# Optimization experiments

Hardware: AMD Instinct MI355X
Metric: run time of the kernel (lower is better)

Reference implementation:

```python
import jax, jax.numpy as jnp
import numpy as np

N_NODES = 100000
N_EDGES = 1600000
D_IN, D_H, D_OUT = 256, 128, 128


def setup_inputs() -> dict:
    key = jax.random.key(0)
    ks = jax.random.split(key, 8)
    x = jax.random.normal(ks[0], (N_NODES, D_IN), dtype=jnp.float32)
    edge_index = jax.random.randint(ks[1], (2, N_EDGES), 0, N_NODES, dtype=jnp.int64)
    def glorot(k, fan_in, fan_out):
        s = jnp.sqrt(6.0 / (fan_in + fan_out))
        return jax.random.uniform(k, (fan_in, fan_out), jnp.float32, -s, s)
    W1 = glorot(ks[2], D_IN, D_H)
    b1 = jnp.zeros((D_H,), jnp.float32)
    W2 = glorot(ks[3], D_H, D_H)
    b2 = jnp.zeros((D_H,), jnp.float32)
    W3 = glorot(ks[4], D_H, D_OUT)
    b3 = jnp.zeros((D_OUT,), jnp.float32)
    return {"x": x, "edge_index": edge_index,
            "W1": W1, "b1": b1, "W2": W2, "b2": b2, "W3": W3, "b3": b3}


def _gcn_norm(edge_index, n_nodes):
    # PyG GCNConv: add self-loops, symmetric normalization D^-1/2 (A+I) D^-1/2
    loop = jnp.arange(n_nodes, dtype=edge_index.dtype)
    src = jnp.concatenate([edge_index[0], loop])  # source j
    dst = jnp.concatenate([edge_index[1], loop])  # target i
    deg = jax.ops.segment_sum(jnp.ones_like(dst, dtype=jnp.float32), dst,
                              num_segments=n_nodes)
    dinv = jnp.where(deg > 0, jax.lax.rsqrt(deg), 0.0)
    norm = dinv[src] * dinv[dst]  # [E+N]
    return src, dst, norm


def _gcn_conv(h, W, b, src, dst, norm, n_nodes):
    h = h @ W                                   # [N, d_out] transform first
    msg = h[src] * norm[:, None]                # gather + edge-weight
    out = jax.ops.segment_sum(msg, dst, num_segments=n_nodes)  # scatter-add
    return out + b


def reference(x, edge_index, W1, b1, W2, b2, W3, b3):
    n = x.shape[0]
    src, dst, norm = _gcn_norm(edge_index, n)
    h = jax.nn.relu(_gcn_conv(x, W1, b1, src, dst, norm, n))
    h = jax.nn.relu(_gcn_conv(h, W2, b2, src, dst, norm, n))
    return _gcn_conv(h, W3, b3, src, dst, norm, n)
```

## Files before the change

### kernel.cpp

```cpp
#include <hip/hip_runtime.h>
#include <hip/hip_fp16.h>
#include <math.h>


#define N_NODES 100000
#define N_EDGES 1600000

typedef _Float16 f16x8 __attribute__((ext_vector_type(8)));
typedef float    f32x4 __attribute__((ext_vector_type(4)));


__global__ __launch_bounds__(256) void k_zero_int(int* __restrict__ p, int n) {
    int i = blockIdx.x * 256 + threadIdx.x;
    if (i < n) p[i] = 0;
}

__global__ __launch_bounds__(256) void k_count(const int* __restrict__ dst, int* __restrict__ cnt, int E) {
    int e = blockIdx.x * 256 + threadIdx.x;
    if (e < E) atomicAdd(&cnt[dst[e]], 1);
}

__global__ __launch_bounds__(256) void k_scan_block(const int* __restrict__ cnt, int* __restrict__ excl,
                                                    int* __restrict__ bsum, int n) {
    __shared__ int s[256];
    int i = blockIdx.x * 256 + threadIdx.x;
    int v = (i < n) ? ((cnt[i] + 7) & ~7) : 0;
    s[threadIdx.x] = v;
    __syncthreads();
    #pragma unroll
    for (int off = 1; off < 256; off <<= 1) {
        int t = (threadIdx.x >= (unsigned)off) ? s[threadIdx.x - off] : 0;
        __syncthreads();
        s[threadIdx.x] += t;
        __syncthreads();
    }
    if (i < n) excl[i] = s[threadIdx.x] - v;
    if (threadIdx.x == 255) bsum[blockIdx.x] = s[255];
}

__global__ __launch_bounds__(512) void k_scan_partials(int* __restrict__ bsum, int nb) {
    __shared__ int s[512];
    int tid = threadIdx.x;
    int v = (tid < nb) ? bsum[tid] : 0;
    s[tid] = v;
    __syncthreads();
    #pragma unroll
    for (int off = 1; off < 512; off <<= 1) {
        int t = (tid >= (unsigned)off) ? s[tid - off] : 0;
        __syncthreads();
        s[tid] += t;
        __syncthreads();
    }
    if (tid < nb) bsum[tid] = s[tid] - v;
}

__global__ __launch_bounds__(256) void k_finalize(const int* __restrict__ excl, const int* __restrict__ bsum,
                                                  const int* __restrict__ cnt, int* __restrict__ rowptr,
                                                  int* __restrict__ fill, float* __restrict__ dinv, int n) {
    int i = blockIdx.x * 256 + threadIdx.x;
    if (i < n) {
        int rp = excl[i] + bsum[i >> 8];
        rowptr[i] = rp;
        fill[i]   = rp;
        dinv[i]   = rsqrtf((float)(cnt[i] + 1));
    }
}

__global__ __launch_bounds__(256) void k_zero_csr(int2* __restrict__ csr, int n) {
    int i = blockIdx.x * 256 + threadIdx.x;
    if (i < n) csr[i] = make_int2(0, 0);
}

__global__ __launch_bounds__(256) void k_fill_edges(const int* __restrict__ src, const int* __restrict__ dst,
                                                    const float* __restrict__ dinv, int* __restrict__ fill,
                                                    int2* __restrict__ csr, int E) {
    int e = blockIdx.x * 256 + threadIdx.x;
    if (e < E) {
        int s = src[e], d = dst[e];
        int p = atomicAdd(&fill[d], 1);
        csr[p] = make_int2(s, __float_as_int(dinv[s] * dinv[d]));
    }
}

__global__ __launch_bounds__(256) void k_wpack(const float* __restrict__ W, _Float16* __restrict__ Wpk, int K) {
    int j = blockIdx.x * 256 + threadIdx.x;
    if (j < K * 128) {
        int i  = j & 7;
        int l  = (j >> 3) & 63;
        int tc = (j >> 9) & 7;
        int c  = j >> 12;
        int col = tc * 16 + (l & 15);
        int k   = c * 32 + (l >> 4) * 8 + i;
        float w = W[(size_t)k * 128 + col];
        _Float16 h = (_Float16)w;
        Wpk[j] = h;
        Wpk[(size_t)K * 128 + j] = (_Float16)(w - (float)h);
    }
}


template <int K>
__global__ __launch_bounds__(256, 3) void k_gemm_mfma(const float* __restrict__ X,
                                                      const _Float16* __restrict__ Wpk,
                                                      _Float16* __restrict__ Y, int n) {
    const int t    = threadIdx.x;
    const int wave = t >> 6;
    const int lane = t & 63;
    const int lrow = lane & 15;
    const int kgrp = lane >> 4;
    const int row0 = blockIdx.x * 64 + wave * 16;
    const int arow = row0 + lrow;
    const bool rok = arow < n;
    const float* __restrict__ xrow = X + (size_t)arow * K;
    const _Float16* __restrict__ Wlo = Wpk + (size_t)K * 128;

    f32x4 acc[8];
    #pragma unroll
    for (int i = 0; i < 8; ++i) acc[i] = (f32x4){0.f, 0.f, 0.f, 0.f};

    #pragma unroll
    for (int c = 0; c < K / 32; ++c) {
        const int k0 = c * 32 + kgrp * 8;
        float4 x0 = make_float4(0.f, 0.f, 0.f, 0.f);
        float4 x1 = make_float4(0.f, 0.f, 0.f, 0.f);
        if (rok) {
            x0 = *(const float4*)&xrow[k0];
            x1 = *(const float4*)&xrow[k0 + 4];
        }
        float xs[8] = {x0.x, x0.y, x0.z, x0.w, x1.x, x1.y, x1.z, x1.w};
        f16x8 ah, al;
        #pragma unroll
        for (int i = 0; i < 8; ++i) {
            _Float16 h = (_Float16)xs[i];
            ah[i] = h;
            al[i] = (_Float16)(xs[i] - (float)h);
        }
        const size_t wb = ((size_t)(c * 8) * 64 + lane) * 8;
        #pragma unroll
        for (int tc = 0; tc < 8; ++tc) {
            f16x8 bh = *(const f16x8*)(Wpk + wb + (size_t)tc * 512);
            f16x8 bl = *(const f16x8*)(Wlo + wb + (size_t)tc * 512);
            acc[tc] = __builtin_amdgcn_mfma_f32_16x16x32_f16(ah, bh, acc[tc], 0, 0, 0);
            acc[tc] = __builtin_amdgcn_mfma_f32_16x16x32_f16(al, bh, acc[tc], 0, 0, 0);
            acc[tc] = __builtin_amdgcn_mfma_f32_16x16x32_f16(ah, bl, acc[tc], 0, 0, 0);
        }
    }

    #pragma unroll
    for (int r = 0; r < 4; ++r) {
        int grow = row0 + kgrp * 4 + r;
        if (grow < n) {
            _Float16* yr = Y + (size_t)grow * 128 + lrow;
            #pragma unroll
            for (int tc = 0; tc < 8; ++tc) yr[tc * 16] = (_Float16)acc[tc][r];
        }
    }
}


template <bool RELU>
__global__ __launch_bounds__(256) void k_agg(const __half* __restrict__ H, const int* __restrict__ rowptr,
                                             const int* __restrict__ cnt, const int2* __restrict__ csr,
                                             const float* __restrict__ dinv, const float* __restrict__ bias,
                                             float* __restrict__ out, int n) {
    const int lane  = threadIdx.x & 63;
    const int wave0 = (int)((blockIdx.x * 256 + threadIdx.x) >> 6);
    const int nwave = (int)((gridDim.x * 256) >> 6);
    const unsigned int* __restrict__ Hu = (const unsigned int*)H;
    const float2 b = *(const float2*)&bias[lane * 2];

    for (int node = wave0; node < n; node += nwave) {
        float dv = dinv[node];
        unsigned int hu = Hu[(size_t)node * 64 + lane];
        float2 h = __half22float2(*(__half2*)&hu);
        float w0 = dv * dv;
        float ax = fmaf(w0, h.x, b.x);
        float ay = fmaf(w0, h.y, b.y);

        const int c0 = rowptr[node];
        const int cn = cnt[node];
        #pragma unroll 2
        for (int e8 = 0; e8 < cn; e8 += 8) {
            const int4* q = (const int4*)(csr + c0 + e8);
            int4 q0 = q[0], q1 = q[1], q2 = q[2], q3 = q[3];
            unsigned int u0 = Hu[(size_t)q0.x * 64 + lane];
            unsigned int u1 = Hu[(size_t)q0.z * 64 + lane];
            unsigned int u2 = Hu[(size_t)q1.x * 64 + lane];
            unsigned int u3 = Hu[(size_t)q1.z * 64 + lane];
            unsigned int u4 = Hu[(size_t)q2.x * 64 + lane];
            unsigned int u5 = Hu[(size_t)q2.z * 64 + lane];
            unsigned int u6 = Hu[(size_t)q3.x * 64 + lane];
            unsigned int u7 = Hu[(size_t)q3.z * 64 + lane];
            float2 g0 = __half22float2(*(__half2*)&u0);
            float2 g1 = __half22float2(*(__half2*)&u1);
            float2 g2 = __half22float2(*(__half2*)&u2);
            float2 g3 = __half22float2(*(__half2*)&u3);
            float2 g4 = __half22float2(*(__half2*)&u4);
            float2 g5 = __half22float2(*(__half2*)&u5);
            float2 g6 = __half22float2(*(__half2*)&u6);
            float2 g7 = __half22float2(*(__half2*)&u7);
            float w0_ = __int_as_float(q0.y), w1_ = __int_as_float(q0.w);
            float w2_ = __int_as_float(q1.y), w3_ = __int_as_float(q1.w);
            float w4_ = __int_as_float(q2.y), w5_ = __int_as_float(q2.w);
            float w6_ = __int_as_float(q3.y), w7_ = __int_as_float(q3.w);
            ax = fmaf(w0_, g0.x, ax); ay = fmaf(w0_, g0.y, ay);
            ax = fmaf(w1_, g1.x, ax); ay = fmaf(w1_, g1.y, ay);
            ax = fmaf(w2_, g2.x, ax); ay = fmaf(w2_, g2.y, ay);
            ax = fmaf(w3_, g3.x, ax); ay = fmaf(w3_, g3.y, ay);
            ax = fmaf(w4_, g4.x, ax); ay = fmaf(w4_, g4.y, ay);
            ax = fmaf(w5_, g5.x, ax); ay = fmaf(w5_, g5.y, ay);
            ax = fmaf(w6_, g6.x, ax); ay = fmaf(w6_, g6.y, ay);
            ax = fmaf(w7_, g7.x, ax); ay = fmaf(w7_, g7.y, ay);
        }

        if (RELU) {
            ax = fmaxf(ax, 0.f);
            ay = fmaxf(ay, 0.f);
        }
        *(float2*)&out[(size_t)node * 128 + lane * 2] = make_float2(ax, ay);
    }
}


extern "C" void kernel_launch(void* const* d_in, const int* in_sizes, int n_in,
                              void* d_out, int out_size, void* d_ws, size_t ws_size,
                              hipStream_t stream) {
    const float* x  = (const float*)d_in[0];
    const int*   ei = (const int*)d_in[1];
    const float* W1 = (const float*)d_in[2];
    const float* b1 = (const float*)d_in[3];
    const float* W2 = (const float*)d_in[4];
    const float* b2 = (const float*)d_in[5];
    const float* W3 = (const float*)d_in[6];
    const float* b3 = (const float*)d_in[7];
    float* out = (float*)d_out;

    const int N = N_NODES, E = N_EDGES;
    const int EP = E + 7 * N + 64;
    const int* src = ei;
    const int* dst = ei + E;

    char* w = (char*)d_ws;
    auto alloc = [&](size_t bytes) -> void* {
        void* p = (void*)w;
        w += (bytes + 255) & ~(size_t)255;
        return p;
    };
    int*      cnt    = (int*)alloc((size_t)N * 4);
    int*      excl   = (int*)alloc((size_t)N * 4);
    int*      bsum   = (int*)alloc(4096);
    int*      rowptr = (int*)alloc((size_t)N * 4);
    int*      fill   = (int*)alloc((size_t)N * 4);
    float*    dinv   = (float*)alloc((size_t)N * 4);
    int2*     csr    = (int2*)alloc((size_t)EP * 8);
    _Float16* Ph     = (_Float16*)alloc((size_t)N * 128 * 2);
    _Float16* Wpk    = (_Float16*)alloc((size_t)2 * 256 * 128 * 2);
    float*    Q      = out;

    const int nbN = (N + 255) / 256;
    const int nbE = (E + 255) / 256;
    const int nbP = (EP + 255) / 256;

    k_zero_int<<<nbN, 256, 0, stream>>>(cnt, N);
    k_count<<<nbE, 256, 0, stream>>>(dst, cnt, E);
    k_scan_block<<<nbN, 256, 0, stream>>>(cnt, excl, bsum, N);
    k_scan_partials<<<1, 512, 0, stream>>>(bsum, nbN);
    k_finalize<<<nbN, 256, 0, stream>>>(excl, bsum, cnt, rowptr, fill, dinv, N);
    k_zero_csr<<<nbP, 256, 0, stream>>>(csr, EP);
    k_fill_edges<<<nbE, 256, 0, stream>>>(src, dst, dinv, fill, csr, E);

    const int gemm_grid = (N + 63) / 64;
    const int agg_grid  = 2048;

    k_wpack<<<(256 * 128 + 255) / 256, 256, 0, stream>>>(W1, Wpk, 256);
    k_gemm_mfma<256><<<gemm_grid, 256, 0, stream>>>(x, Wpk, Ph, N);
    k_agg<true><<<agg_grid, 256, 0, stream>>>((const __half*)Ph, rowptr, cnt, csr, dinv, b1, Q, N);
    k_wpack<<<(128 * 128 + 255) / 256, 256, 0, stream>>>(W2, Wpk, 128);
    k_gemm_mfma<128><<<gemm_grid, 256, 0, stream>>>(Q, Wpk, Ph, N);
    k_agg<true><<<agg_grid, 256, 0, stream>>>((const __half*)Ph, rowptr, cnt, csr, dinv, b2, Q, N);
    k_wpack<<<(128 * 128 + 255) / 256, 256, 0, stream>>>(W3, Wpk, 128);
    k_gemm_mfma<128><<<gemm_grid, 256, 0, stream>>>(Q, Wpk, Ph, N);
    k_agg<false><<<agg_grid, 256, 0, stream>>>((const __half*)Ph, rowptr, cnt, csr, dinv, b3, out, N);
}
```

Before: 470.1 us.

## Split CSR fill into destination ranges and process two nodes per wave in aggregation

The aggregation kernel now assigns two destination nodes to each wave, one per half-wave, and each lane handles four features with 8-byte loads and 16-byte stores instead of two. Each wave therefore issues twice as many independent gathers and needs fewer loop trips per node, but the two halves can diverge when their degrees differ. The edge fill now runs as four passes, each handling only edges whose destination falls in a quarter of the node range. This keeps the atomic counters and CSR writes of each pass within a smaller window to improve cache locality, at the cost of reading the edge list four times. The aggregation pairing assumes an even node count, which holds for N=100000.

```diff
diff --git a/kernel.cpp b/kernel.cpp
--- a/kernel.cpp
+++ b/kernel.cpp
@@ -73,12 +73,15 @@
 
 __global__ __launch_bounds__(256) void k_fill_edges(const int* __restrict__ src, const int* __restrict__ dst,
                                                     const float* __restrict__ dinv, int* __restrict__ fill,
-                                                    int2* __restrict__ csr, int E) {
+                                                    int2* __restrict__ csr, int E, int lo, int hi) {
     int e = blockIdx.x * 256 + threadIdx.x;
     if (e < E) {
-        int s = src[e], d = dst[e];
-        int p = atomicAdd(&fill[d], 1);
-        csr[p] = make_int2(s, __float_as_int(dinv[s] * dinv[d]));
+        int d = dst[e];
+        if (d >= lo && d < hi) {
+            int s = src[e];
+            int p = atomicAdd(&fill[d], 1);
+            csr[p] = make_int2(s, __float_as_int(dinv[s] * dinv[d]));
+        }
     }
 }
 
@@ -164,60 +167,92 @@
                                              const float* __restrict__ dinv, const float* __restrict__ bias,
                                              float* __restrict__ out, int n) {
     const int lane  = threadIdx.x & 63;
+    const int half  = lane >> 5;
+    const int sl    = lane & 31;
     const int wave0 = (int)((blockIdx.x * 256 + threadIdx.x) >> 6);
     const int nwave = (int)((gridDim.x * 256) >> 6);
-    const unsigned int* __restrict__ Hu = (const unsigned int*)H;
-    const float2 b = *(const float2*)&bias[lane * 2];
-
-    for (int node = wave0; node < n; node += nwave) {
+    const uint2* __restrict__ Hu = (const uint2*)H;
+    const float4 b = *(const float4*)&bias[sl * 4];
+
+    const int npair = n >> 1;
+    for (int p = wave0; p < npair; p += nwave) {
+        const int node = p * 2 + half;
         float dv = dinv[node];
-        unsigned int hu = Hu[(size_t)node * 64 + lane];
-        float2 h = __half22float2(*(__half2*)&hu);
+        uint2 hu = Hu[(size_t)node * 32 + sl];
+        float2 f01 = __half22float2(*(__half2*)&hu.x);
+        float2 f23 = __half22float2(*(__half2*)&hu.y);
         float w0 = dv * dv;
-        float ax = fmaf(w0, h.x, b.x);
-        float ay = fmaf(w0, h.y, b.y);
+        float ax = fmaf(w0, f01.x, b.x);
+        float ay = fmaf(w0, f01.y, b.y);
+        float az = fmaf(w0, f23.x, b.z);
+        float aw = fmaf(w0, f23.y, b.w);
 
         const int c0 = rowptr[node];
         const int cn = cnt[node];
-        #pragma unroll 2
         for (int e8 = 0; e8 < cn; e8 += 8) {
             const int4* q = (const int4*)(csr + c0 + e8);
             int4 q0 = q[0], q1 = q[1], q2 = q[2], q3 = q[3];
-            unsigned int u0 = Hu[(size_t)q0.x * 64 + lane];
-            unsigned int u1 = Hu[(size_t)q0.z * 64 + lane];
-            unsigned int u2 = Hu[(size_t)q1.x * 64 + lane];
-            unsigned int u3 = Hu[(size_t)q1.z * 64 + lane];
-            unsigned int u4 = Hu[(size_t)q2.x * 64 + lane];
-            unsigned int u5 = Hu[(size_t)q2.z * 64 + lane];
-            unsigned int u6 = Hu[(size_t)q3.x * 64 + lane];
-            unsigned int u7 = Hu[(size_t)q3.z * 64 + lane];
-            float2 g0 = __half22float2(*(__half2*)&u0);
-            float2 g1 = __half22float2(*(__half2*)&u1);
-            float2 g2 = __half22float2(*(__half2*)&u2);
-            float2 g3 = __half22float2(*(__half2*)&u3);
-            float2 g4 = __half22float2(*(__half2*)&u4);
-            float2 g5 = __half22float2(*(__half2*)&u5);
-            float2 g6 = __half22float2(*(__half2*)&u6);
-            float2 g7 = __half22float2(*(__half2*)&u7);
+            uint2 u0 = Hu[(size_t)q0.x * 32 + sl];
+            uint2 u1 = Hu[(size_t)q0.z * 32 + sl];
+            uint2 u2 = Hu[(size_t)q1.x * 32 + sl];
+            uint2 u3 = Hu[(size_t)q1.z * 32 + sl];
+            uint2 u4 = Hu[(size_t)q2.x * 32 + sl];
+            uint2 u5 = Hu[(size_t)q2.z * 32 + sl];
+            uint2 u6 = Hu[(size_t)q3.x * 32 + sl];
+            uint2 u7 = Hu[(size_t)q3.z * 32 + sl];
             float w0_ = __int_as_float(q0.y), w1_ = __int_as_float(q0.w);
             float w2_ = __int_as_float(q1.y), w3_ = __int_as_float(q1.w);
             float w4_ = __int_as_float(q2.y), w5_ = __int_as_float(q2.w);
             float w6_ = __int_as_float(q3.y), w7_ = __int_as_float(q3.w);
-            ax = fmaf(w0_, g0.x, ax); ay = fmaf(w0_, g0.y, ay);
-            ax = fmaf(w1_, g1.x, ax); ay = fmaf(w1_, g1.y, ay);
-            ax = fmaf(w2_, g2.x, ax); ay = fmaf(w2_, g2.y, ay);
-            ax = fmaf(w3_, g3.x, ax); ay = fmaf(w3_, g3.y, ay);
-            ax = fmaf(w4_, g4.x, ax); ay = fmaf(w4_, g4.y, ay);
-            ax = fmaf(w5_, g5.x, ax); ay = fmaf(w5_, g5.y, ay);
-            ax = fmaf(w6_, g6.x, ax); ay = fmaf(w6_, g6.y, ay);
-            ax = fmaf(w7_, g7.x, ax); ay = fmaf(w7_, g7.y, ay);
+            {
+                float2 a01 = __half22float2(*(__half2*)&u0.x), a23 = __half22float2(*(__half2*)&u0.y);
+                ax = fmaf(w0_, a01.x, ax); ay = fmaf(w0_, a01.y, ay);
+                az = fmaf(w0_, a23.x, az); aw = fmaf(w0_, a23.y, aw);
+            }
+            {
+                float2 a01 = __half22float2(*(__half2*)&u1.x), a23 = __half22float2(*(__half2*)&u1.y);
+                ax = fmaf(w1_, a01.x, ax); ay = fmaf(w1_, a01.y, ay);
+                az = fmaf(w1_, a23.x, az); aw = fmaf(w1_, a23.y, aw);
+            }
+            {
+                float2 a01 = __half22float2(*(__half2*)&u2.x), a23 = __half22float2(*(__half2*)&u2.y);
+                ax = fmaf(w2_, a01.x, ax); ay = fmaf(w2_, a01.y, ay);
+                az = fmaf(w2_, a23.x, az); aw = fmaf(w2_, a23.y, aw);
+            }
+            {
+                float2 a01 = __half22float2(*(__half2*)&u3.x), a23 = __half22float2(*(__half2*)&u3.y);
+                ax = fmaf(w3_, a01.x, ax); ay = fmaf(w3_, a01.y, ay);
+                az = fmaf(w3_, a23.x, az); aw = fmaf(w3_, a23.y, aw);
+            }
+            {
+                float2 a01 = __half22float2(*(__half2*)&u4.x), a23 = __half22float2(*(__half2*)&u4.y);
+                ax = fmaf(w4_, a01.x, ax); ay = fmaf(w4_, a01.y, ay);
+                az = fmaf(w4_, a23.x, az); aw = fmaf(w4_, a23.y, aw);
+            }
+            {
+                float2 a01 = __half22float2(*(__half2*)&u5.x), a23 = __half22float2(*(__half2*)&u5.y);
+                ax = fmaf(w5_, a01.x, ax); ay = fmaf(w5_, a01.y, ay);
+                az = fmaf(w5_, a23.x, az); aw = fmaf(w5_, a23.y, aw);
+            }
+            {
+                float2 a01 = __half22float2(*(__half2*)&u6.x), a23 = __half22float2(*(__half2*)&u6.y);
+                ax = fmaf(w6_, a01.x, ax); ay = fmaf(w6_, a01.y, ay);
+                az = fmaf(w6_, a23.x, az); aw = fmaf(w6_, a23.y, aw);
+            }
+            {
+                float2 a01 = __half22float2(*(__half2*)&u7.x), a23 = __half22float2(*(__half2*)&u7.y);
+                ax = fmaf(w7_, a01.x, ax); ay = fmaf(w7_, a01.y, ay);
+                az = fmaf(w7_, a23.x, az); aw = fmaf(w7_, a23.y, aw);
+            }
         }
 
         if (RELU) {
             ax = fmaxf(ax, 0.f);
             ay = fmaxf(ay, 0.f);
-        }
-        *(float2*)&out[(size_t)node * 128 + lane * 2] = make_float2(ax, ay);
+            az = fmaxf(az, 0.f);
+            aw = fmaxf(aw, 0.f);
+        }
+        *(float4*)&out[(size_t)node * 128 + sl * 4] = make_float4(ax, ay, az, aw);
     }
 }
 
@@ -267,7 +302,11 @@
     k_scan_partials<<<1, 512, 0, stream>>>(bsum, nbN);
     k_finalize<<<nbN, 256, 0, stream>>>(excl, bsum, cnt, rowptr, fill, dinv, N);
     k_zero_csr<<<nbP, 256, 0, stream>>>(csr, EP);
-    k_fill_edges<<<nbE, 256, 0, stream>>>(src, dst, dinv, fill, csr, E);
+    for (int r = 0; r < 4; ++r) {
+        int lo = r * (N / 4);
+        int hi = (r == 3) ? N : (r + 1) * (N / 4);
+        k_fill_edges<<<nbE, 256, 0, stream>>>(src, dst, dinv, fill, csr, E, lo, hi);
+    }
 
     const int gemm_grid = (N + 63) / 64;
     const int agg_grid  = 2048;
```

Result: slower. 501.9 us (+6.8%).

## Fold symmetric norm into GEMM rows, shrink CSR to src-only, quad-node aggregation

Applied to the files above, without the earlier changes.

The per-edge normalization dinv[s]*dinv[d] is factored out: the GEMM epilogue scales each output row by dinv of its node, and the aggregation applies dinv of the destination once at the end. The CSR therefore stores only source indices, padded with a dummy node whose zeroed row absorbs padding, which halves edge-index traffic. Aggregation now handles four nodes per wave with 16-byte feature loads per lane. The GEMM stages X through swizzled shared memory with register prefetch of the next K chunk. This adds barriers and relies on padding-row zeroing and n being a multiple of four.

```diff
diff --git a/kernel.cpp b/kernel.cpp
--- a/kernel.cpp
+++ b/kernel.cpp
@@ -66,19 +66,19 @@
     }
 }
 
-__global__ __launch_bounds__(256) void k_zero_csr(int2* __restrict__ csr, int n) {
+__global__ __launch_bounds__(256) void k_init_csr(int* __restrict__ csr, int n, unsigned int* __restrict__ phz) {
     int i = blockIdx.x * 256 + threadIdx.x;
-    if (i < n) csr[i] = make_int2(0, 0);
+    if (i < n) csr[i] = N_NODES;
+    if (blockIdx.x == 0 && threadIdx.x < 64) phz[threadIdx.x] = 0;
 }
 
 __global__ __launch_bounds__(256) void k_fill_edges(const int* __restrict__ src, const int* __restrict__ dst,
-                                                    const float* __restrict__ dinv, int* __restrict__ fill,
-                                                    int2* __restrict__ csr, int E) {
+                                                    int* __restrict__ fill, int* __restrict__ csr, int E) {
     int e = blockIdx.x * 256 + threadIdx.x;
     if (e < E) {
-        int s = src[e], d = dst[e];
+        int d = dst[e];
         int p = atomicAdd(&fill[d], 1);
-        csr[p] = make_int2(s, __float_as_int(dinv[s] * dinv[d]));
+        csr[p] = src[e];
     }
 }
 
@@ -100,33 +100,49 @@
 
 
 template <int K>
-__global__ __launch_bounds__(256, 3) void k_gemm_mfma(const float* __restrict__ X,
-                                                      const _Float16* __restrict__ Wpk,
-                                                      _Float16* __restrict__ Y, int n) {
+__global__ __launch_bounds__(256) void k_gemm_mfma(const float* __restrict__ X,
+                                                   const _Float16* __restrict__ Wpk,
+                                                   const float* __restrict__ dinv,
+                                                   _Float16* __restrict__ Y, int n) {
+    constexpr int NC = K / 32;
+    __shared__ float sX[64 * 32];
     const int t    = threadIdx.x;
     const int wave = t >> 6;
     const int lane = t & 63;
     const int lrow = lane & 15;
     const int kgrp = lane >> 4;
-    const int row0 = blockIdx.x * 64 + wave * 16;
-    const int arow = row0 + lrow;
-    const bool rok = arow < n;
-    const float* __restrict__ xrow = X + (size_t)arow * K;
+    const int row0 = blockIdx.x * 64;
+    const int R    = wave * 16 + lrow;
     const _Float16* __restrict__ Wlo = Wpk + (size_t)K * 128;
 
+    const int rs0 = t >> 3,        gs = t & 7;
+    const int rs1 = (t >> 3) + 32;
+    const int gc0 = (gs ^ (rs0 & 7)) << 2;
+    const int gc1 = (gs ^ (rs1 & 7)) << 2;
+    const int gr0 = row0 + rs0, gr1 = row0 + rs1;
+    const bool ok0 = gr0 < n, ok1 = gr1 < n;
+    const float* __restrict__ xr0 = X + (size_t)gr0 * K;
+    const float* __restrict__ xr1 = X + (size_t)gr1 * K;
+
     f32x4 acc[8];
     #pragma unroll
     for (int i = 0; i < 8; ++i) acc[i] = (f32x4){0.f, 0.f, 0.f, 0.f};
 
-    #pragma unroll
-    for (int c = 0; c < K / 32; ++c) {
-        const int k0 = c * 32 + kgrp * 8;
-        float4 x0 = make_float4(0.f, 0.f, 0.f, 0.f);
-        float4 x1 = make_float4(0.f, 0.f, 0.f, 0.f);
-        if (rok) {
-            x0 = *(const float4*)&xrow[k0];
-            x1 = *(const float4*)&xrow[k0 + 4];
-        }
+    const float4 z4 = make_float4(0.f, 0.f, 0.f, 0.f);
+    float4 rv0 = ok0 ? *(const float4*)&xr0[gc0] : z4;
+    float4 rv1 = ok1 ? *(const float4*)&xr1[gc1] : z4;
+    *(float4*)&sX[(rs0 * 8 + gs) * 4] = rv0;
+    *(float4*)&sX[(rs1 * 8 + gs) * 4] = rv1;
+    __syncthreads();
+
+    #pragma unroll
+    for (int c = 0; c < NC; ++c) {
+        if (c + 1 < NC) {
+            rv0 = ok0 ? *(const float4*)&xr0[(c + 1) * 32 + gc0] : z4;
+            rv1 = ok1 ? *(const float4*)&xr1[(c + 1) * 32 + gc1] : z4;
+        }
+        float4 x0 = *(const float4*)&sX[(R * 8 + ((kgrp * 2)     ^ (R & 7))) * 4];
+        float4 x1 = *(const float4*)&sX[(R * 8 + ((kgrp * 2 + 1) ^ (R & 7))) * 4];
         float xs[8] = {x0.x, x0.y, x0.z, x0.w, x1.x, x1.y, x1.z, x1.w};
         f16x8 ah, al;
         #pragma unroll
@@ -144,80 +160,93 @@
             acc[tc] = __builtin_amdgcn_mfma_f32_16x16x32_f16(al, bh, acc[tc], 0, 0, 0);
             acc[tc] = __builtin_amdgcn_mfma_f32_16x16x32_f16(ah, bl, acc[tc], 0, 0, 0);
         }
+        if (c + 1 < NC) {
+            __syncthreads();
+            *(float4*)&sX[(rs0 * 8 + gs) * 4] = rv0;
+            *(float4*)&sX[(rs1 * 8 + gs) * 4] = rv1;
+            __syncthreads();
+        }
     }
 
     #pragma unroll
     for (int r = 0; r < 4; ++r) {
-        int grow = row0 + kgrp * 4 + r;
+        int grow = row0 + wave * 16 + kgrp * 4 + r;
         if (grow < n) {
+            float dv = dinv[grow];
             _Float16* yr = Y + (size_t)grow * 128 + lrow;
             #pragma unroll
-            for (int tc = 0; tc < 8; ++tc) yr[tc * 16] = (_Float16)acc[tc][r];
-        }
-    }
-}
-
+            for (int tc = 0; tc < 8; ++tc) yr[tc * 16] = (_Float16)(dv * acc[tc][r]);
+        }
+    }
+}
+
+
+__device__ __forceinline__ void acc8(float a[8], uint4 u) {
+    float2 p;
+    p = __half22float2(*(__half2*)&u.x); a[0] += p.x; a[1] += p.y;
+    p = __half22float2(*(__half2*)&u.y); a[2] += p.x; a[3] += p.y;
+    p = __half22float2(*(__half2*)&u.z); a[4] += p.x; a[5] += p.y;
+    p = __half22float2(*(__half2*)&u.w); a[6] += p.x; a[7] += p.y;
+}
 
 template <bool RELU>
 __global__ __launch_bounds__(256) void k_agg(const __half* __restrict__ H, const int* __restrict__ rowptr,
-                                             const int* __restrict__ cnt, const int2* __restrict__ csr,
+                                             const int* __restrict__ cnt, const int* __restrict__ csr,
                                              const float* __restrict__ dinv, const float* __restrict__ bias,
                                              float* __restrict__ out, int n) {
     const int lane  = threadIdx.x & 63;
+    const int q     = lane >> 4;
+    const int fl    = lane & 15;
     const int wave0 = (int)((blockIdx.x * 256 + threadIdx.x) >> 6);
     const int nwave = (int)((gridDim.x * 256) >> 6);
-    const unsigned int* __restrict__ Hu = (const unsigned int*)H;
-    const float2 b = *(const float2*)&bias[lane * 2];
-
-    for (int node = wave0; node < n; node += nwave) {
-        float dv = dinv[node];
-        unsigned int hu = Hu[(size_t)node * 64 + lane];
-        float2 h = __half22float2(*(__half2*)&hu);
-        float w0 = dv * dv;
-        float ax = fmaf(w0, h.x, b.x);
-        float ay = fmaf(w0, h.y, b.y);
+    const uint4* __restrict__ Hu = (const uint4*)H;
+    const float4 b0 = *(const float4*)&bias[fl * 8];
+    const float4 b1 = *(const float4*)&bias[fl * 8 + 4];
+
+    const int nquad = n >> 2;
+    for (int g = wave0; g < nquad; g += nwave) {
+        const int node = g * 4 + q;
+        float a[8];
+        {
+            uint4 u = Hu[(size_t)node * 16 + fl];
+            float2 p;
+            p = __half22float2(*(__half2*)&u.x); a[0] = p.x; a[1] = p.y;
+            p = __half22float2(*(__half2*)&u.y); a[2] = p.x; a[3] = p.y;
+            p = __half22float2(*(__half2*)&u.z); a[4] = p.x; a[5] = p.y;
+            p = __half22float2(*(__half2*)&u.w); a[6] = p.x; a[7] = p.y;
+        }
 
         const int c0 = rowptr[node];
         const int cn = cnt[node];
-        #pragma unroll 2
         for (int e8 = 0; e8 < cn; e8 += 8) {
-            const int4* q = (const int4*)(csr + c0 + e8);
-            int4 q0 = q[0], q1 = q[1], q2 = q[2], q3 = q[3];
-            unsigned int u0 = Hu[(size_t)q0.x * 64 + lane];
-            unsigned int u1 = Hu[(size_t)q0.z * 64 + lane];
-            unsigned int u2 = Hu[(size_t)q1.x * 64 + lane];
-            unsigned int u3 = Hu[(size_t)q1.z * 64 + lane];
-            unsigned int u4 = Hu[(size_t)q2.x * 64 + lane];
-            unsigned int u5 = Hu[(size_t)q2.z * 64 + lane];
-            unsigned int u6 = Hu[(size_t)q3.x * 64 + lane];
-            unsigned int u7 = Hu[(size_t)q3.z * 64 + lane];
-            float2 g0 = __half22float2(*(__half2*)&u0);
-            float2 g1 = __half22float2(*(__half2*)&u1);
-            float2 g2 = __half22float2(*(__half2*)&u2);
-            float2 g3 = __half22float2(*(__half2*)&u3);
-            float2 g4 = __half22float2(*(__half2*)&u4);
-            float2 g5 = __half22float2(*(__half2*)&u5);
-            float2 g6 = __half22float2(*(__half2*)&u6);
-            float2 g7 = __half22float2(*(__half2*)&u7);
-            float w0_ = __int_as_float(q0.y), w1_ = __int_as_float(q0.w);
-            float w2_ = __int_as_float(q1.y), w3_ = __int_as_float(q1.w);
-            float w4_ = __int_as_float(q2.y), w5_ = __int_as_float(q2.w);
-            float w6_ = __int_as_float(q3.y), w7_ = __int_as_float(q3.w);
-            ax = fmaf(w0_, g0.x, ax); ay = fmaf(w0_, g0.y, ay);
-            ax = fmaf(w1_, g1.x, ax); ay = fmaf(w1_, g1.y, ay);
-            ax = fmaf(w2_, g2.x, ax); ay = fmaf(w2_, g2.y, ay);
-            ax = fmaf(w3_, g3.x, ax); ay = fmaf(w3_, g3.y, ay);
-            ax = fmaf(w4_, g4.x, ax); ay = fmaf(w4_, g4.y, ay);
-            ax = fmaf(w5_, g5.x, ax); ay = fmaf(w5_, g5.y, ay);
-            ax = fmaf(w6_, g6.x, ax); ay = fmaf(w6_, g6.y, ay);
-            ax = fmaf(w7_, g7.x, ax); ay = fmaf(w7_, g7.y, ay);
-        }
-
+            const int4* qp = (const int4*)(csr + c0 + e8);
+            int4 qa = qp[0], qb = qp[1];
+            uint4 u0 = Hu[(size_t)qa.x * 16 + fl];
+            uint4 u1 = Hu[(size_t)qa.y * 16 + fl];
+            uint4 u2 = Hu[(size_t)qa.z * 16 + fl];
+            uint4 u3 = Hu[(size_t)qa.w * 16 + fl];
+            uint4 u4 = Hu[(size_t)qb.x * 16 + fl];
+            uint4 u5 = Hu[(size_t)qb.y * 16 + fl];
+            uint4 u6 = Hu[(size_t)qb.z * 16 + fl];
+            uint4 u7 = Hu[(size_t)qb.w * 16 + fl];
+            acc8(a, u0); acc8(a, u1); acc8(a, u2); acc8(a, u3);
+            acc8(a, u4); acc8(a, u5); acc8(a, u6); acc8(a, u7);
+        }
+
+        const float dv = dinv[node];
+        float4 o0, o1;
+        o0.x = fmaf(dv, a[0], b0.x); o0.y = fmaf(dv, a[1], b0.y);
+        o0.z = fmaf(dv, a[2], b0.z); o0.w = fmaf(dv, a[3], b0.w);
+        o1.x = fmaf(dv, a[4], b1.x); o1.y = fmaf(dv, a[5], b1.y);
+        o1.z = fmaf(dv, a[6], b1.z); o1.w = fmaf(dv, a[7], b1.w);
         if (RELU) {
-            ax = fmaxf(ax, 0.f);
-            ay = fmaxf(ay, 0.f);
-        }
-        *(float2*)&out[(size_t)node * 128 + lane * 2] = make_float2(ax, ay);
+            o0.x = fmaxf(o0.x, 0.f); o0.y = fmaxf(o0.y, 0.f);
+            o0.z = fmaxf(o0.z, 0.f); o0.w = fmaxf(o0.w, 0.f);
+            o1.x = fmaxf(o1.x, 0.f); o1.y = fmaxf(o1.y, 0.f);
+            o1.z = fmaxf(o1.z, 0.f); o1.w = fmaxf(o1.w, 0.f);
+        }
+        *(float4*)&out[(size_t)node * 128 + fl * 8]     = o0;
+        *(float4*)&out[(size_t)node * 128 + fl * 8 + 4] = o1;
     }
 }
 
@@ -252,8 +281,8 @@
     int*      rowptr = (int*)alloc((size_t)N * 4);
     int*      fill   = (int*)alloc((size_t)N * 4);
     float*    dinv   = (float*)alloc((size_t)N * 4);
-    int2*     csr    = (int2*)alloc((size_t)EP * 8);
-    _Float16* Ph     = (_Float16*)alloc((size_t)N * 128 * 2);
+    int*      csr    = (int*)alloc((size_t)EP * 4);
+    _Float16* Ph     = (_Float16*)alloc((size_t)(N + 8) * 128 * 2);
     _Float16* Wpk    = (_Float16*)alloc((size_t)2 * 256 * 128 * 2);
     float*    Q      = out;
 
@@ -266,19 +295,19 @@
     k_scan_block<<<nbN, 256, 0, stream>>>(cnt, excl, bsum, N);
     k_scan_partials<<<1, 512, 0, stream>>>(bsum, nbN);
     k_finalize<<<nbN, 256, 0, stream>>>(excl, bsum, cnt, rowptr, fill, dinv, N);
-    k_zero_csr<<<nbP, 256, 0, stream>>>(csr, EP);
-    k_fill_edges<<<nbE, 256, 0, stream>>>(src, dst, dinv, fill, csr, E);
+    k_init_csr<<<nbP, 256, 0, stream>>>(csr, EP, (unsigned int*)(Ph + (size_t)N * 128));
+    k_fill_edges<<<nbE, 256, 0, stream>>>(src, dst, fill, csr, E);
 
     const int gemm_grid = (N + 63) / 64;
     const int agg_grid  = 2048;
 
     k_wpack<<<(256 * 128 + 255) / 256, 256, 0, stream>>>(W1, Wpk, 256);
-    k_gemm_mfma<256><<<gemm_grid, 256, 0, stream>>>(x, Wpk, Ph, N);
+    k_gemm_mfma<256><<<gemm_grid, 256, 0, stream>>>(x, Wpk, dinv, Ph, N);
     k_agg<true><<<agg_grid, 256, 0, stream>>>((const __half*)Ph, rowptr, cnt, csr, dinv, b1, Q, N);
     k_wpack<<<(128 * 128 + 255) / 256, 256, 0, stream>>>(W2, Wpk, 128);
-    k_gemm_mfma<128><<<gemm_grid, 256, 0, stream>>>(Q, Wpk, Ph, N);
+    k_gemm_mfma<128><<<gemm_grid, 256, 0, stream>>>(Q, Wpk, dinv, Ph, N);
     k_agg<true><<<agg_grid, 256, 0, stream>>>((const __half*)Ph, rowptr, cnt, csr, dinv, b2, Q, N);
     k_wpack<<<(128 * 128 + 255) / 256, 256, 0, stream>>>(W3, Wpk, 128);
-    k_gemm_mfma<128><<<gemm_grid, 256, 0, stream>>>(Q, Wpk, Ph, N);
+    k_gemm_mfma<128><<<gemm_grid, 256, 0, stream>>>(Q, Wpk, dinv, Ph, N);
     k_agg<false><<<agg_grid, 256, 0, stream>>>((const __half*)Ph, rowptr, cnt, csr, dinv, b3, out, N);
 }
```

New measurement: 491.4 us. 4.5% more time.
